# Optimization experiments

Hardware: AMD Instinct MI355X
Metric: run time of the kernel (lower is better)

Reference implementation:

```python
import jax, jax.numpy as jnp
import numpy as np

N = 50000
E = 640000
F_IN = 128
F_OUT = 128


def setup_inputs() -> dict:
    key = jax.random.key(0)
    k1, k2, k3, k4, k5 = jax.random.split(key, 5)
    x = jax.random.normal(k1, (N, F_IN), dtype=jnp.float32)
    edge_index = jax.random.randint(k2, (2, E), 0, N, dtype=jnp.int64)
    s = 1.0 / np.sqrt(F_IN)
    W_l = jax.random.uniform(k3, (F_IN, F_OUT), minval=-s, maxval=s, dtype=jnp.float32)
    W_r = jax.random.uniform(k4, (F_IN, F_OUT), minval=-s, maxval=s, dtype=jnp.float32)
    b = jax.random.uniform(k5, (F_OUT,), minval=-s, maxval=s, dtype=jnp.float32)
    return {"x": x, "edge_index": edge_index, "W_l": W_l, "W_r": W_r, "b": b}


def reference(x, edge_index, W_l, W_r, b):
    src, dst = edge_index[0], edge_index[1]
    # gather source-node features along edges: [E, F_in]
    msgs = x[src]
    # mean aggregation at destination nodes
    summed = jax.ops.segment_sum(msgs, dst, num_segments=N)          # [N, F_in]
    counts = jax.ops.segment_sum(jnp.ones((E,), jnp.float32), dst, num_segments=N)
    mean_nb = summed / jnp.maximum(counts, 1.0)[:, None]
    # SAGEConv: lin_l(aggregated) + lin_r(self), bias on lin_l only
    out = mean_nb @ W_l + x @ W_r + b
    return jax.nn.relu(out)
```

## Files before the change

### kernel.cpp

```cpp
#include <hip/hip_runtime.h>

#define N_NODES 50000
#define E_EDGES 640000
#define F 128

typedef __attribute__((ext_vector_type(8))) short short8;
typedef __attribute__((ext_vector_type(4))) float f32x4;

#define DEG_OFF 0
#define OFF_OFF 200704
#define CUR_OFF 401408
#define BSUM_OFF 601600
#define WF_OFF 603648
#define SRC_OFF 734720
#define XBF_OFF 3294720
#define MBF_OFF 16094720
#define WS_NEED_FULL 28894720ULL

#define FILL_BLKS 2048
#define WPREP_BLKS 16
#define XCAST_BLKS 3125
#define FXW_GRID (FILL_BLKS + WPREP_BLKS + XCAST_BLKS)

__device__ __forceinline__ unsigned short f2bf(float f) {
    unsigned int u = __builtin_bit_cast(unsigned int, f);
    u += 0x7FFFu + ((u >> 16) & 1u);
    return (unsigned short)(u >> 16);
}
__device__ __forceinline__ float bfhi2f(unsigned int hi16) {
    return __builtin_bit_cast(float, hi16 & 0xFFFF0000u);
}

__global__ __launch_bounds__(256) void gnn_hist(const int* __restrict__ ei,
                                                int* __restrict__ deg) {
    const int i = blockIdx.x * blockDim.x + threadIdx.x;
    const int stride = gridDim.x * blockDim.x;
    for (int e = i; e < E_EDGES; e += stride)
        atomicAdd(&deg[ei[E_EDGES + e]], 1);
}

__global__ __launch_bounds__(256) void gnn_scan_a(const int* __restrict__ deg,
                                                  int* __restrict__ off,
                                                  int* __restrict__ bsum) {
    __shared__ int s[256];
    const int t = threadIdx.x;
    const int i = blockIdx.x * 256 + t;
    const int v = (i < N_NODES) ? deg[i] : 0;
    s[t] = v;
    __syncthreads();
    for (int d = 1; d < 256; d <<= 1) {
        const int u = (t >= d) ? s[t - d] : 0;
        __syncthreads();
        s[t] += u;
        __syncthreads();
    }
    if (i < N_NODES) off[i] = s[t] - v;
    if (t == 255) bsum[blockIdx.x] = s[255];
}

__global__ __launch_bounds__(256) void gnn_scan2(const int* __restrict__ bsum,
                                                 int* __restrict__ off,
                                                 int* __restrict__ cur) {
    __shared__ int s[256];
    const int t = threadIdx.x;
    const int bid = blockIdx.x;
    s[t] = (t < 196) ? bsum[t] : 0;
    __syncthreads();
    for (int d = 1; d < 256; d <<= 1) {
        const int u = (t >= d) ? s[t - d] : 0;
        __syncthreads();
        s[t] += u;
        __syncthreads();
    }
    const int myPre = (bid == 0) ? 0 : s[bid - 1];
    const int i = bid * 256 + t;
    if (i < N_NODES) {
        const int o = off[i] + myPre;
        off[i] = o;
        cur[i] = o;
    }
    if (bid == 0 && t == 0) off[N_NODES] = s[195];
}

__global__ __launch_bounds__(256) void gnn_fill_xw(
    const int* __restrict__ ei, int* __restrict__ cur, int* __restrict__ srcs,
    const float* __restrict__ x, const float* __restrict__ Wl,
    const float* __restrict__ Wr, short* __restrict__ Wf,
    unsigned short* __restrict__ xbf, int full) {
    const int bid = blockIdx.x;
    const int t = threadIdx.x;
    if (bid < FILL_BLKS) {
        const int i = bid * 256 + t;
        const int stride = FILL_BLKS * 256;
        for (int e = i; e < E_EDGES; e += stride) {
            const int d = ei[E_EDGES + e];
            const int p = atomicAdd(&cur[d], 1);
            srcs[p] = ei[e];
        }
    } else if (bid < FILL_BLKS + WPREP_BLKS) {
        const int tid = (bid - FILL_BLKS) * 256 + t;
        const int lane = tid & 63;
        const int frag = tid >> 6;
        const int kstep = frag >> 3;
        const int ct = frag & 7;
        const int kb = kstep * 32 + (lane >> 4) * 8;
        const int c = ct * 16 + (lane & 15);
        short8 v;
#pragma unroll
        for (int j = 0; j < 8; ++j) {
            const int k = kb + j;
            const float f = (k < F) ? Wl[k * F + c] : Wr[(k - F) * F + c];
            v[j] = (short)f2bf(f);
        }
        *reinterpret_cast<short8*>(Wf + (size_t)tid * 8) = v;
    } else {
        if (!full) return;
        const size_t i =
            ((size_t)(bid - FILL_BLKS - WPREP_BLKS) * 256 + t) * 8;
        const float4 a0 = *reinterpret_cast<const float4*>(x + i);
        const float4 a1 = *reinterpret_cast<const float4*>(x + i + 4);
        short8 v;
        v[0] = (short)f2bf(a0.x); v[1] = (short)f2bf(a0.y);
        v[2] = (short)f2bf(a0.z); v[3] = (short)f2bf(a0.w);
        v[4] = (short)f2bf(a1.x); v[5] = (short)f2bf(a1.y);
        v[6] = (short)f2bf(a1.z); v[7] = (short)f2bf(a1.w);
        *reinterpret_cast<short8*>((short*)xbf + i) = v;
    }
}

#define ACCQ(u, A0, A1)                                        \
    A0[0] += bfhi2f(u.x << 16); A0[1] += bfhi2f(u.x);          \
    A0[2] += bfhi2f(u.y << 16); A0[3] += bfhi2f(u.y);          \
    A1[0] += bfhi2f(u.z << 16); A1[1] += bfhi2f(u.z);          \
    A1[2] += bfhi2f(u.w << 16); A1[3] += bfhi2f(u.w);

__global__ __launch_bounds__(256) void gnn_aggregate_bf(
    const unsigned short* __restrict__ xbf, const int* __restrict__ off,
    const int* __restrict__ srcs, unsigned short* __restrict__ mbf) {
    const int node = blockIdx.x * 4 + (threadIdx.x >> 6);
    if (node >= N_NODES) return;
    const int lane = threadIdx.x & 63;
    const int grp = lane >> 4;
    const int l16 = lane & 15;
    const int o0 = off[node];
    const int o1 = off[node + 1];
    const unsigned short* xb = xbf + l16 * 8;
    f32x4 a0 = {0.f, 0.f, 0.f, 0.f}, a1 = {0.f, 0.f, 0.f, 0.f};
    f32x4 b0 = {0.f, 0.f, 0.f, 0.f}, b1 = {0.f, 0.f, 0.f, 0.f};
    int j = o0;
    for (; j + 8 <= o1; j += 8) {
        const uint4 u =
            *reinterpret_cast<const uint4*>(xb + (size_t)srcs[j + grp] * F);
        const uint4 v =
            *reinterpret_cast<const uint4*>(xb + (size_t)srcs[j + 4 + grp] * F);
        ACCQ(u, a0, a1);
        ACCQ(v, b0, b1);
    }
    if (j + 4 <= o1) {
        const uint4 u =
            *reinterpret_cast<const uint4*>(xb + (size_t)srcs[j + grp] * F);
        ACCQ(u, a0, a1);
        j += 4;
    }
    if (j < o1) {
        const int jj = j + grp;
        const uint4 u = *reinterpret_cast<const uint4*>(
            xb + (size_t)srcs[(jj < o1) ? jj : o0] * F);
        if (jj < o1) { ACCQ(u, b0, b1); }
    }
    a0 += b0;
    a1 += b1;
    f32x4 t0, t1;
#pragma unroll
    for (int i = 0; i < 4; ++i) {
        t0[i] = __shfl_xor(a0[i], 16, 64);
        t1[i] = __shfl_xor(a1[i], 16, 64);
    }
    a0 += t0; a1 += t1;
#pragma unroll
    for (int i = 0; i < 4; ++i) {
        t0[i] = __shfl_xor(a0[i], 32, 64);
        t1[i] = __shfl_xor(a1[i], 32, 64);
    }
    a0 += t0; a1 += t1;
    if (grp == 0) {
        const float inv = 1.0f / (float)max(o1 - o0, 1);
        a0 *= inv; a1 *= inv;
        uint4 m;
        m.x = (unsigned)f2bf(a0[0]) | ((unsigned)f2bf(a0[1]) << 16);
        m.y = (unsigned)f2bf(a0[2]) | ((unsigned)f2bf(a0[3]) << 16);
        m.z = (unsigned)f2bf(a1[0]) | ((unsigned)f2bf(a1[1]) << 16);
        m.w = (unsigned)f2bf(a1[2]) | ((unsigned)f2bf(a1[3]) << 16);
        *reinterpret_cast<uint4*>(mbf + (size_t)node * F + l16 * 8) = m;
    }
}

__global__ __launch_bounds__(256) void gnn_finalize_bf(
    const unsigned short* __restrict__ xbf, const unsigned short* __restrict__ mbf,
    const short* __restrict__ Wf, const float* __restrict__ bias,
    float* __restrict__ out) {
    const int t = threadIdx.x;
    const int lane = t & 63;
    const int wv = t >> 6;
    const int r0 = blockIdx.x * 64 + wv * 16;
    const int rl = lane & 15;
    const int kg = lane >> 4;
    const int arow = r0 + rl;
    const int arow_c = (arow < N_NODES) ? arow : (N_NODES - 1);

    f32x4 acc[8];
#pragma unroll
    for (int ct = 0; ct < 8; ++ct) acc[ct] = (f32x4){0.f, 0.f, 0.f, 0.f};

#pragma unroll
    for (int kstep = 0; kstep < 8; ++kstep) {
        const int k0 = kstep * 32 + kg * 8;
        const unsigned short* asrc =
            (kstep < 4) ? (mbf + (size_t)arow_c * F + k0)
                        : (xbf + (size_t)arow_c * F + (k0 - F));
        const short8 af = *reinterpret_cast<const short8*>(asrc);
#pragma unroll
        for (int ct = 0; ct < 8; ++ct) {
            const short8 bf = *reinterpret_cast<const short8*>(
                Wf + (size_t)((kstep * 8 + ct) * 64 + lane) * 8);
            acc[ct] = __builtin_amdgcn_mfma_f32_16x16x32_bf16(af, bf, acc[ct],
                                                              0, 0, 0);
        }
    }

#pragma unroll
    for (int ct = 0; ct < 8; ++ct) {
        const int c = ct * 16 + rl;
        const float bv = bias[c];
#pragma unroll
        for (int r = 0; r < 4; ++r) {
            const int row = r0 + kg * 4 + r;
            if (row < N_NODES)
                out[(size_t)row * F + c] = fmaxf(acc[ct][r] + bv, 0.0f);
        }
    }
}

__global__ __launch_bounds__(256) void gnn_aggregate(
    const float* __restrict__ x, const int* __restrict__ off,
    const int* __restrict__ srcs, float* __restrict__ out) {
    const int node = blockIdx.x * 4 + (threadIdx.x >> 6);
    if (node >= N_NODES) return;
    const int lane = threadIdx.x & 63;
    const int half = lane >> 5;
    const int l32 = lane & 31;
    const int o0 = off[node];
    const int o1 = off[node + 1];
    f32x4 acc0 = {0.f, 0.f, 0.f, 0.f};
    f32x4 acc1 = {0.f, 0.f, 0.f, 0.f};
    int j = o0;
    for (; j + 4 <= o1; j += 4) {
        const int sA = srcs[j + half];
        const int sB = srcs[j + 2 + half];
        acc0 += *reinterpret_cast<const f32x4*>(x + (size_t)sA * F + l32 * 4);
        acc1 += *reinterpret_cast<const f32x4*>(x + (size_t)sB * F + l32 * 4);
    }
    for (; j < o1; j += 2) {
        const int jj = j + half;
        const int s = srcs[(jj < o1) ? jj : o0];
        f32x4 v = *reinterpret_cast<const f32x4*>(x + (size_t)s * F + l32 * 4);
        if (jj >= o1) v = (f32x4){0.f, 0.f, 0.f, 0.f};
        acc0 += v;
    }
    acc0 += acc1;
    f32x4 o;
    o[0] = __shfl_xor(acc0[0], 32, 64);
    o[1] = __shfl_xor(acc0[1], 32, 64);
    o[2] = __shfl_xor(acc0[2], 32, 64);
    o[3] = __shfl_xor(acc0[3], 32, 64);
    acc0 += o;
    if (half == 0) {
        const float inv = 1.0f / (float)max(o1 - o0, 1);
        acc0 *= inv;
        *reinterpret_cast<f32x4*>(out + (size_t)node * F + l32 * 4) = acc0;
    }
}

__global__ __launch_bounds__(256) void gnn_finalize_mfma(
    const float* __restrict__ x, const short* __restrict__ Wf,
    const float* __restrict__ bias, float* __restrict__ out) {
    const int t = threadIdx.x;
    const int lane = t & 63;
    const int wv = t >> 6;
    const int r0 = blockIdx.x * 64 + wv * 16;
    const int rl = lane & 15;
    const int kg = lane >> 4;
    const int arow = r0 + rl;
    const int arow_c = (arow < N_NODES) ? arow : (N_NODES - 1);
    f32x4 acc[8];
#pragma unroll
    for (int ct = 0; ct < 8; ++ct) acc[ct] = (f32x4){0.f, 0.f, 0.f, 0.f};
#pragma unroll
    for (int kstep = 0; kstep < 8; ++kstep) {
        const int k0 = kstep * 32 + kg * 8;
        const float* asrc = (kstep < 4) ? (out + (size_t)arow_c * F + k0)
                                        : (x + (size_t)arow_c * F + (k0 - F));
        const float4 a0 = *reinterpret_cast<const float4*>(asrc);
        const float4 a1 = *reinterpret_cast<const float4*>(asrc + 4);
        short8 af;
        af[0] = (short)f2bf(a0.x); af[1] = (short)f2bf(a0.y);
        af[2] = (short)f2bf(a0.z); af[3] = (short)f2bf(a0.w);
        af[4] = (short)f2bf(a1.x); af[5] = (short)f2bf(a1.y);
        af[6] = (short)f2bf(a1.z); af[7] = (short)f2bf(a1.w);
#pragma unroll
        for (int ct = 0; ct < 8; ++ct) {
            const short8 bf = *reinterpret_cast<const short8*>(
                Wf + (size_t)((kstep * 8 + ct) * 64 + lane) * 8);
            acc[ct] = __builtin_amdgcn_mfma_f32_16x16x32_bf16(af, bf, acc[ct],
                                                              0, 0, 0);
        }
    }
#pragma unroll
    for (int ct = 0; ct < 8; ++ct) {
        const int c = ct * 16 + rl;
        const float bv = bias[c];
#pragma unroll
        for (int r = 0; r < 4; ++r) {
            const int row = r0 + kg * 4 + r;
            if (row < N_NODES)
                out[(size_t)row * F + c] = fmaxf(acc[ct][r] + bv, 0.0f);
        }
    }
}

extern "C" void kernel_launch(void* const* d_in, const int* in_sizes, int n_in,
                              void* d_out, int out_size, void* d_ws,
                              size_t ws_size, hipStream_t stream) {
    const float* x = (const float*)d_in[0];
    const int* ei = (const int*)d_in[1];
    const float* Wl = (const float*)d_in[2];
    const float* Wr = (const float*)d_in[3];
    const float* b = (const float*)d_in[4];
    float* out = (float*)d_out;

    char* ws = (char*)d_ws;
    int* deg = (int*)(ws + DEG_OFF);
    int* off = (int*)(ws + OFF_OFF);
    int* cur = (int*)(ws + CUR_OFF);
    int* bsum = (int*)(ws + BSUM_OFF);
    short* Wf = (short*)(ws + WF_OFF);
    int* srcs = (int*)(ws + SRC_OFF);
    unsigned short* xbf = (unsigned short*)(ws + XBF_OFF);
    unsigned short* mbf = (unsigned short*)(ws + MBF_OFF);

    const int full = (ws_size >= WS_NEED_FULL) ? 1 : 0;

    hipMemsetAsync(deg, 0, N_NODES * sizeof(int), stream);
    gnn_hist<<<2048, 256, 0, stream>>>(ei, deg);
    gnn_scan_a<<<196, 256, 0, stream>>>(deg, off, bsum);
    gnn_scan2<<<196, 256, 0, stream>>>(bsum, off, cur);
    gnn_fill_xw<<<FXW_GRID, 256, 0, stream>>>(ei, cur, srcs, x, Wl, Wr, Wf,
                                              xbf, full);

    if (full) {
        gnn_aggregate_bf<<<(N_NODES + 3) / 4, 256, 0, stream>>>(xbf, off, srcs,
                                                                mbf);
        gnn_finalize_bf<<<(N_NODES + 63) / 64, 256, 0, stream>>>(xbf, mbf, Wf,
                                                                 b, out);
    } else {
        gnn_aggregate<<<(N_NODES + 3) / 4, 256, 0, stream>>>(x, off, srcs, out);
        gnn_finalize_mfma<<<(N_NODES + 63) / 64, 256, 0, stream>>>(x, Wf, b,
                                                                   out);
    }
}
```

Measured before the change: 201.0 us.

## Partition CSR fill by XCD, store 16-bit source indices, move casts into histogram kernel

Moves the bf16 cast of x and the weight fragment prep into the histogram kernel. The CSR fill kernel is left doing only the edge scatter. The fill is split into eight destination-node ranges selected by blockIdx & 7, so the atomics on cur for a given node come from blocks that round-robin placement puts on the same XCD, keeping them in one L2. Source indices are stored as 16-bit values, which is valid because the node count is below 65536, and this halves index traffic in the scatter and aggregation. The cost is that every partition rereads the whole destination array, so edge-index reads grow eightfold.

```diff
diff --git a/kernel.cpp b/kernel.cpp
--- a/kernel.cpp
+++ b/kernel.cpp
@@ -3,6 +3,8 @@
 #define N_NODES 50000
 #define E_EDGES 640000
 #define F 128
+#define NXCD 8
+#define NPER (N_NODES / NXCD)
 
 typedef __attribute__((ext_vector_type(8))) short short8;
 typedef __attribute__((ext_vector_type(4))) float f32x4;
@@ -17,10 +19,11 @@
 #define MBF_OFF 16094720
 #define WS_NEED_FULL 28894720ULL
 
+#define XCAST_BLKS 3125
+#define WPREP_BLKS 16
+#define HIST_BLKS 2048
+#define PREP_GRID (XCAST_BLKS + WPREP_BLKS + HIST_BLKS)
 #define FILL_BLKS 2048
-#define WPREP_BLKS 16
-#define XCAST_BLKS 3125
-#define FXW_GRID (FILL_BLKS + WPREP_BLKS + XCAST_BLKS)
 
 __device__ __forceinline__ unsigned short f2bf(float f) {
     unsigned int u = __builtin_bit_cast(unsigned int, f);
@@ -31,12 +34,46 @@
     return __builtin_bit_cast(float, hi16 & 0xFFFF0000u);
 }
 
-__global__ __launch_bounds__(256) void gnn_hist(const int* __restrict__ ei,
-                                                int* __restrict__ deg) {
-    const int i = blockIdx.x * blockDim.x + threadIdx.x;
-    const int stride = gridDim.x * blockDim.x;
-    for (int e = i; e < E_EDGES; e += stride)
-        atomicAdd(&deg[ei[E_EDGES + e]], 1);
+__global__ __launch_bounds__(256) void gnn_prep(
+    const float* __restrict__ x, const int* __restrict__ ei,
+    const float* __restrict__ Wl, const float* __restrict__ Wr,
+    short* __restrict__ Wf, unsigned short* __restrict__ xbf,
+    int* __restrict__ deg, int full) {
+    const int bid = blockIdx.x;
+    const int t = threadIdx.x;
+    if (bid < XCAST_BLKS) {
+        if (!full) return;
+        const size_t i = ((size_t)bid * 256 + t) * 8;
+        const float4 a0 = *reinterpret_cast<const float4*>(x + i);
+        const float4 a1 = *reinterpret_cast<const float4*>(x + i + 4);
+        short8 v;
+        v[0] = (short)f2bf(a0.x); v[1] = (short)f2bf(a0.y);
+        v[2] = (short)f2bf(a0.z); v[3] = (short)f2bf(a0.w);
+        v[4] = (short)f2bf(a1.x); v[5] = (short)f2bf(a1.y);
+        v[6] = (short)f2bf(a1.z); v[7] = (short)f2bf(a1.w);
+        *reinterpret_cast<short8*>((short*)xbf + i) = v;
+    } else if (bid < XCAST_BLKS + WPREP_BLKS) {
+        const int tid = (bid - XCAST_BLKS) * 256 + t;
+        const int lane = tid & 63;
+        const int frag = tid >> 6;
+        const int kstep = frag >> 3;
+        const int ct = frag & 7;
+        const int kb = kstep * 32 + (lane >> 4) * 8;
+        const int c = ct * 16 + (lane & 15);
+        short8 v;
+#pragma unroll
+        for (int j = 0; j < 8; ++j) {
+            const int k = kb + j;
+            const float f = (k < F) ? Wl[k * F + c] : Wr[(k - F) * F + c];
+            v[j] = (short)f2bf(f);
+        }
+        *reinterpret_cast<short8*>(Wf + (size_t)tid * 8) = v;
+    } else {
+        const int i = (bid - XCAST_BLKS - WPREP_BLKS) * 256 + t;
+        const int stride = HIST_BLKS * 256;
+        for (int e = i; e < E_EDGES; e += stride)
+            atomicAdd(&deg[ei[E_EDGES + e]], 1);
+    }
 }
 
 __global__ __launch_bounds__(256) void gnn_scan_a(const int* __restrict__ deg,
@@ -82,49 +119,21 @@
     if (bid == 0 && t == 0) off[N_NODES] = s[195];
 }
 
-__global__ __launch_bounds__(256) void gnn_fill_xw(
-    const int* __restrict__ ei, int* __restrict__ cur, int* __restrict__ srcs,
-    const float* __restrict__ x, const float* __restrict__ Wl,
-    const float* __restrict__ Wr, short* __restrict__ Wf,
-    unsigned short* __restrict__ xbf, int full) {
-    const int bid = blockIdx.x;
-    const int t = threadIdx.x;
-    if (bid < FILL_BLKS) {
-        const int i = bid * 256 + t;
-        const int stride = FILL_BLKS * 256;
-        for (int e = i; e < E_EDGES; e += stride) {
-            const int d = ei[E_EDGES + e];
+__global__ __launch_bounds__(256) void gnn_fill(
+    const int* __restrict__ ei, int* __restrict__ cur,
+    unsigned short* __restrict__ srcs) {
+    const int grp = blockIdx.x & (NXCD - 1);
+    const int g = blockIdx.x >> 3;
+    const int lo = grp * NPER;
+    const int hi = lo + NPER;
+    const int i = g * 256 + threadIdx.x;
+    const int stride = (FILL_BLKS / NXCD) * 256;
+    for (int e = i; e < E_EDGES; e += stride) {
+        const int d = ei[E_EDGES + e];
+        if (d >= lo && d < hi) {
             const int p = atomicAdd(&cur[d], 1);
-            srcs[p] = ei[e];
-        }
-    } else if (bid < FILL_BLKS + WPREP_BLKS) {
-        const int tid = (bid - FILL_BLKS) * 256 + t;
-        const int lane = tid & 63;
-        const int frag = tid >> 6;
-        const int kstep = frag >> 3;
-        const int ct = frag & 7;
-        const int kb = kstep * 32 + (lane >> 4) * 8;
-        const int c = ct * 16 + (lane & 15);
-        short8 v;
-#pragma unroll
-        for (int j = 0; j < 8; ++j) {
-            const int k = kb + j;
-            const float f = (k < F) ? Wl[k * F + c] : Wr[(k - F) * F + c];
-            v[j] = (short)f2bf(f);
-        }
-        *reinterpret_cast<short8*>(Wf + (size_t)tid * 8) = v;
-    } else {
-        if (!full) return;
-        const size_t i =
-            ((size_t)(bid - FILL_BLKS - WPREP_BLKS) * 256 + t) * 8;
-        const float4 a0 = *reinterpret_cast<const float4*>(x + i);
-        const float4 a1 = *reinterpret_cast<const float4*>(x + i + 4);
-        short8 v;
-        v[0] = (short)f2bf(a0.x); v[1] = (short)f2bf(a0.y);
-        v[2] = (short)f2bf(a0.z); v[3] = (short)f2bf(a0.w);
-        v[4] = (short)f2bf(a1.x); v[5] = (short)f2bf(a1.y);
-        v[6] = (short)f2bf(a1.z); v[7] = (short)f2bf(a1.w);
-        *reinterpret_cast<short8*>((short*)xbf + i) = v;
+            srcs[p] = (unsigned short)ei[e];
+        }
     }
 }
 
@@ -136,7 +145,7 @@
 
 __global__ __launch_bounds__(256) void gnn_aggregate_bf(
     const unsigned short* __restrict__ xbf, const int* __restrict__ off,
-    const int* __restrict__ srcs, unsigned short* __restrict__ mbf) {
+    const unsigned short* __restrict__ srcs, unsigned short* __restrict__ mbf) {
     const int node = blockIdx.x * 4 + (threadIdx.x >> 6);
     if (node >= N_NODES) return;
     const int lane = threadIdx.x & 63;
@@ -149,16 +158,16 @@
     f32x4 b0 = {0.f, 0.f, 0.f, 0.f}, b1 = {0.f, 0.f, 0.f, 0.f};
     int j = o0;
     for (; j + 8 <= o1; j += 8) {
-        const uint4 u =
-            *reinterpret_cast<const uint4*>(xb + (size_t)srcs[j + grp] * F);
-        const uint4 v =
-            *reinterpret_cast<const uint4*>(xb + (size_t)srcs[j + 4 + grp] * F);
+        const uint4 u = *reinterpret_cast<const uint4*>(
+            xb + (size_t)srcs[j + grp] * F);
+        const uint4 v = *reinterpret_cast<const uint4*>(
+            xb + (size_t)srcs[j + 4 + grp] * F);
         ACCQ(u, a0, a1);
         ACCQ(v, b0, b1);
     }
     if (j + 4 <= o1) {
-        const uint4 u =
-            *reinterpret_cast<const uint4*>(xb + (size_t)srcs[j + grp] * F);
+        const uint4 u = *reinterpret_cast<const uint4*>(
+            xb + (size_t)srcs[j + grp] * F);
         ACCQ(u, a0, a1);
         j += 4;
     }
@@ -243,7 +252,7 @@
 
 __global__ __launch_bounds__(256) void gnn_aggregate(
     const float* __restrict__ x, const int* __restrict__ off,
-    const int* __restrict__ srcs, float* __restrict__ out) {
+    const unsigned short* __restrict__ srcs, float* __restrict__ out) {
     const int node = blockIdx.x * 4 + (threadIdx.x >> 6);
     if (node >= N_NODES) return;
     const int lane = threadIdx.x & 63;
@@ -344,18 +353,17 @@
     int* cur = (int*)(ws + CUR_OFF);
     int* bsum = (int*)(ws + BSUM_OFF);
     short* Wf = (short*)(ws + WF_OFF);
-    int* srcs = (int*)(ws + SRC_OFF);
+    unsigned short* srcs = (unsigned short*)(ws + SRC_OFF);
     unsigned short* xbf = (unsigned short*)(ws + XBF_OFF);
     unsigned short* mbf = (unsigned short*)(ws + MBF_OFF);
 
     const int full = (ws_size >= WS_NEED_FULL) ? 1 : 0;
 
     hipMemsetAsync(deg, 0, N_NODES * sizeof(int), stream);
-    gnn_hist<<<2048, 256, 0, stream>>>(ei, deg);
+    gnn_prep<<<PREP_GRID, 256, 0, stream>>>(x, ei, Wl, Wr, Wf, xbf, deg, full);
     gnn_scan_a<<<196, 256, 0, stream>>>(deg, off, bsum);
     gnn_scan2<<<196, 256, 0, stream>>>(bsum, off, cur);
-    gnn_fill_xw<<<FXW_GRID, 256, 0, stream>>>(ei, cur, srcs, x, Wl, Wr, Wf,
-                                              xbf, full);
+    gnn_fill<<<FILL_BLKS, 256, 0, stream>>>(ei, cur, srcs);
 
     if (full) {
         gnn_aggregate_bf<<<(N_NODES + 3) / 4, 256, 0, stream>>>(xbf, off, srcs,
```

After: 192.5 us. 1.04x faster.
